# Performance work log

Hardware: AMD Instinct MI355X
Metric: run time of the kernel (lower is better)

## Reference

```python
import jax, jax.numpy as jnp
import numpy as np

B, SEQ, D = 2, 1024, 768
E, H = 8, 3072          # num_experts, expert hidden (mlp_ratio=4)
CAPACITY = 2            # k = CAPACITY * num_tokens


def setup_inputs() -> dict:
    key = jax.random.key(0)
    ks = jax.random.split(key, 6)
    x = jax.random.normal(ks[0], (B, SEQ, D), dtype=jnp.float32)
    gate_weight = jax.random.normal(ks[1], (E, D), dtype=jnp.float32) * 0.006
    w1 = jax.random.normal(ks[2], (E, D, H), dtype=jnp.float32) * (1.0 / np.sqrt(D))
    b1 = jnp.zeros((E, H), dtype=jnp.float32)
    w2 = jax.random.normal(ks[3], (E, H, D), dtype=jnp.float32) * (1.0 / np.sqrt(H))
    b2 = jnp.zeros((E, D), dtype=jnp.float32)
    return {"x": x, "gate_weight": gate_weight, "w1": w1, "b1": b1, "w2": w2, "b2": b2}


def reference(x, gate_weight, w1, b1, w2, b2):
    Bb, s, d = x.shape
    xf = x.reshape(-1, d)                     # [S, D]
    S = xf.shape[0]
    k = S * CAPACITY
    logits = xf @ gate_weight.T               # [S, E]
    scores = jax.nn.softmax(logits, axis=-1).T  # [E, S]
    # flattened top-k over all (expert, token) pairs -> sparse gate matrix
    vals, idx = jax.lax.top_k(scores.reshape(-1), k)
    gate = jnp.zeros((E * S,), dtype=x.dtype).at[idx].add(vals).reshape(E, S)
    # expert MLPs (GELU-tanh) applied per expert; zero gate entries kill
    # non-routed (expert, token) pairs -> same math as gather/MLP/scatter.
    h = jax.nn.gelu(jnp.einsum('sd,edh->esh', xf, w1) + b1[:, None, :], approximate=True)
    out = jnp.einsum('esh,ehd->esd', h, w2) + b2[:, None, :]   # [E, S, D]
    y = jnp.einsum('es,esd->sd', gate, out)    # weighted combine + sum over experts
    return y.reshape(Bb, s, d)
```

## Files before the change

kernel.cpp:

```cpp
#include <hip/hip_runtime.h>
#include <math.h>

#define S_TOK 2048
#define NEXP  8
#define DDIM  768
#define HDIM  3072
#define KSEL  4096
#define NT_MAX 40

typedef __attribute__((ext_vector_type(8))) short short8;
typedef __attribute__((ext_vector_type(4))) float f32x4;

__device__ __forceinline__ unsigned short f2bf(float f) {
  unsigned u = __float_as_uint(f);
  u += 0x7fffu + ((u >> 16) & 1u);
  return (unsigned short)(u >> 16);
}

__device__ __forceinline__ float gelu_fast(float v) {
  float u = 0.7978845608028654f * (v + 0.044715f * v * v * v);
  float t = __expf(-2.0f * fabsf(u));
  float th = (1.0f - t) / (1.0f + t);
  th = copysignf(th, u);
  return 0.5f * v * (1.0f + th);
}

__global__ __launch_bounds__(256) void zero_kernel(float* __restrict__ p, int n) {
  int i = blockIdx.x * 256 + threadIdx.x;
  if (i < n) p[i] = 0.f;
}

__global__ __launch_bounds__(256) void convx_kernel(const float* __restrict__ x,
                                                    short* __restrict__ xb) {
  int i = (blockIdx.x * 256 + threadIdx.x) * 8;
  float4 a = *(const float4*)(x + i);
  float4 b = *(const float4*)(x + i + 4);
  short8 v;
  v[0] = (short)f2bf(a.x); v[1] = (short)f2bf(a.y);
  v[2] = (short)f2bf(a.z); v[3] = (short)f2bf(a.w);
  v[4] = (short)f2bf(b.x); v[5] = (short)f2bf(b.y);
  v[6] = (short)f2bf(b.z); v[7] = (short)f2bf(b.w);
  *(short8*)(xb + i) = v;
}

__global__ __launch_bounds__(256) void gate_kernel(
    const float* __restrict__ x, const float* __restrict__ gw,
    float* __restrict__ scores)
{
  int tid  = threadIdx.x;
  int lane = tid & 63;
  int wid  = tid >> 6;
  int token = blockIdx.x * 4 + wid;
  const float* xr = x + (size_t)token * DDIM;

  float acc[NEXP];
#pragma unroll
  for (int e = 0; e < NEXP; ++e) acc[e] = 0.f;

  for (int d = lane; d < DDIM; d += 64) {
    float xv = xr[d];
#pragma unroll
    for (int e = 0; e < NEXP; ++e) acc[e] += xv * gw[e * DDIM + d];
  }
#pragma unroll
  for (int e = 0; e < NEXP; ++e) {
    for (int off = 32; off; off >>= 1) acc[e] += __shfl_down(acc[e], off, 64);
  }
  if (lane == 0) {
    float m = acc[0];
#pragma unroll
    for (int e = 1; e < NEXP; ++e) m = fmaxf(m, acc[e]);
    float p[NEXP], s = 0.f;
#pragma unroll
    for (int e = 0; e < NEXP; ++e) { p[e] = expf(acc[e] - m); s += p[e]; }
    float inv = 1.0f / s;
#pragma unroll
    for (int e = 0; e < NEXP; ++e) scores[e * S_TOK + token] = p[e] * inv;
  }
}

__device__ unsigned block_scan_excl(unsigned v, volatile unsigned* wsum) {
  int tid = threadIdx.x, lane = tid & 63, wid = tid >> 6;
  __syncthreads();
  unsigned x = v;
#pragma unroll
  for (int off = 1; off < 64; off <<= 1) {
    unsigned t = __shfl_up(x, off, 64);
    if (lane >= off) x += t;
  }
  if (lane == 63) wsum[wid] = x;
  __syncthreads();
  if (tid < 64) {
    unsigned w = (lane < 16) ? wsum[lane] : 0u;
#pragma unroll
    for (int off = 1; off < 16; off <<= 1) {
      unsigned t = __shfl_up(w, off, 64);
      if (lane >= off) w += t;
    }
    if (lane < 16) wsum[lane] = w;
  }
  __syncthreads();
  unsigned woff = (wid > 0) ? wsum[wid - 1] : 0u;
  return woff + (x - v);
}

__global__ __launch_bounds__(1024) void select_kernel(
    const float* __restrict__ scores,
    int* __restrict__ tokenlist, float* __restrict__ slotgate,
    int* __restrict__ offsets, int* __restrict__ tilemap)
{
  __shared__ unsigned cnt;
  __shared__ unsigned wsum[16];
  __shared__ int soff[8];
  int tid = threadIdx.x;
  int base = tid * 16;

  float sv[16]; unsigned key[16];
#pragma unroll
  for (int j = 0; j < 16; ++j) {
    sv[j] = scores[base + j];
    key[j] = __float_as_uint(sv[j]);
  }

  unsigned lo = 0, hi = 0x3F800000u;
  while (lo < hi) {
    unsigned mid = lo + ((hi - lo + 1) >> 1);
    if (tid == 0) cnt = 0;
    __syncthreads();
    unsigned c = 0;
#pragma unroll
    for (int j = 0; j < 16; ++j) c += (key[j] >= mid) ? 1u : 0u;
    for (int off = 32; off; off >>= 1) c += __shfl_down(c, off, 64);
    if ((tid & 63) == 0) atomicAdd(&cnt, c);
    __syncthreads();
    unsigned tot = cnt;
    __syncthreads();
    if (tot >= (unsigned)KSEL) lo = mid; else hi = mid - 1;
  }
  unsigned V = lo;

  if (tid == 0) cnt = 0;
  __syncthreads();
  {
    unsigned c = 0;
#pragma unroll
    for (int j = 0; j < 16; ++j) c += (key[j] > V) ? 1u : 0u;
    for (int off = 32; off; off >>= 1) c += __shfl_down(c, off, 64);
    if ((tid & 63) == 0) atomicAdd(&cnt, c);
  }
  __syncthreads();
  int need = KSEL - (int)cnt;
  __syncthreads();

  unsigned tloc = 0;
#pragma unroll
  for (int j = 0; j < 16; ++j) tloc += (key[j] == V) ? 1u : 0u;
  unsigned texcl = block_scan_excl(tloc, wsum);

  unsigned selmask = 0, sloc = 0, trun = texcl;
#pragma unroll
  for (int j = 0; j < 16; ++j) {
    bool f;
    if (key[j] > V) f = true;
    else if (key[j] == V) { f = ((int)trun < need); ++trun; }
    else f = false;
    if (f) { selmask |= (1u << j); ++sloc; }
  }
  unsigned sexcl = block_scan_excl(sloc, wsum);

  if ((tid & 127) == 0) soff[tid >> 7] = (int)sexcl;
  __syncthreads();
  if (tid == 0) {
    int nt = 0;
#pragma unroll
    for (int e = 0; e < NEXP; ++e) {
      offsets[e] = soff[e];
      int rows = ((e == NEXP - 1) ? KSEL : soff[e + 1]) - soff[e];
      int t = (rows + 127) >> 7;
      for (int i = 0; i < t; ++i) tilemap[nt++] = (e << 16) | i;
    }
    offsets[NEXP] = KSEL;
    for (int i = nt; i < NT_MAX; ++i) tilemap[i] = -1;
  }

  unsigned p = sexcl;
#pragma unroll
  for (int j = 0; j < 16; ++j) {
    int i = base + j;
    if (selmask & (1u << j)) {
      tokenlist[p] = i & (S_TOK - 1);
      slotgate[p] = sv[j];
      ++p;
    }
  }
}

template <int MODE>
__global__ __launch_bounds__(256) void moe_mfma(
    const short* __restrict__ Abase, const float* __restrict__ W,
    const float* __restrict__ bias, void* __restrict__ outp,
    const int* __restrict__ offsets, const int* __restrict__ tokenlist,
    const float* __restrict__ slotgate, const int* __restrict__ tilemap,
    int chunk_base, int K, int N, int klen)
{
  const int tinfo = tilemap[chunk_base + blockIdx.y];
  if (tinfo < 0) return;
  const int e = tinfo >> 16;
  const int tloc = tinfo & 0xffff;
  const int r0 = offsets[e];
  const int rows = offsets[e + 1] - r0;
  const int rowbase = tloc << 7;
  int vr = rows - rowbase; if (vr > 128) vr = 128;
  const int colbase = (int)blockIdx.x << 7;
  const int lbuf = (int)blockIdx.y << 7;
  const int split = (int)blockIdx.z;
  const int kb = split * klen;

  __shared__ short Ab[128 * 40];
  __shared__ short Bb[128 * 40];

  const int tid = threadIdx.x;
  const int lane = tid & 63;
  const int wid = tid >> 6;
  const int wr = (wid >> 1) << 6;
  const int wc = (wid & 1) << 6;
  const int l15 = lane & 15;
  const int lq = lane >> 4;

  const int ar = tid >> 1;
  const int ak = (tid & 1) << 4;
  const short* arow;
  {
    int cr = (ar < vr) ? ar : (vr - 1);
    if (MODE == 1) arow = Abase + (size_t)tokenlist[r0 + rowbase + cr] * DDIM;
    else           arow = Abase + (size_t)(lbuf + cr) * HDIM;
  }
  const int bn = tid & 127;
  const int bk = (tid >> 7) << 4;
  const float* wcol = W + (size_t)e * K * N + colbase + bn;

  f32x4 acc[4][4];
#pragma unroll
  for (int i = 0; i < 4; ++i)
#pragma unroll
    for (int j = 0; j < 4; ++j) acc[i][j] = (f32x4){0.f, 0.f, 0.f, 0.f};

  short8 av0, av1;
  float bw[16];
  {
    const short* ap = arow + kb + ak;
    av0 = *(const short8*)(ap);
    av1 = *(const short8*)(ap + 8);
    const float* wp = wcol + (size_t)(kb + bk) * N;
#pragma unroll
    for (int j = 0; j < 16; ++j) bw[j] = wp[(size_t)j * N];
  }

  for (int k0 = 0; k0 < klen; k0 += 32) {
    __syncthreads();
    *(short8*)&Ab[ar * 40 + ak] = av0;
    *(short8*)&Ab[ar * 40 + ak + 8] = av1;
    {
      short8 b0, b1;
#pragma unroll
      for (int j = 0; j < 8; ++j) {
        b0[j] = (short)f2bf(bw[j]);
        b1[j] = (short)f2bf(bw[j + 8]);
      }
      *(short8*)&Bb[bn * 40 + bk] = b0;
      *(short8*)&Bb[bn * 40 + bk + 8] = b1;
    }
    __syncthreads();
    if (k0 + 32 < klen) {
      const short* ap = arow + kb + k0 + 32 + ak;
      av0 = *(const short8*)(ap);
      av1 = *(const short8*)(ap + 8);
      const float* wp = wcol + (size_t)(kb + k0 + 32 + bk) * N;
#pragma unroll
      for (int j = 0; j < 16; ++j) bw[j] = wp[(size_t)j * N];
    }
    short8 af[4], bfr[4];
#pragma unroll
    for (int i = 0; i < 4; ++i)
      af[i] = *(const short8*)&Ab[(wr + i * 16 + l15) * 40 + lq * 8];
#pragma unroll
    for (int j = 0; j < 4; ++j)
      bfr[j] = *(const short8*)&Bb[(wc + j * 16 + l15) * 40 + lq * 8];
#pragma unroll
    for (int i = 0; i < 4; ++i)
#pragma unroll
      for (int j = 0; j < 4; ++j)
        acc[i][j] = __builtin_amdgcn_mfma_f32_16x16x32_bf16(af[i], bfr[j], acc[i][j], 0, 0, 0);
  }

  if (MODE == 1) {
    short* hb = (short*)outp;
    const float* bp = bias + (size_t)e * N + colbase;
#pragma unroll
    for (int i = 0; i < 4; ++i) {
      int rb = wr + i * 16 + lq * 4;
#pragma unroll
      for (int j = 0; j < 4; ++j) {
        int col = wc + j * 16 + l15;
        float bv = bp[col];
#pragma unroll
        for (int p = 0; p < 4; ++p) {
          int r = rb + p;
          if (r < vr)
            hb[(size_t)(lbuf + r) * HDIM + colbase + col] =
                (short)f2bf(gelu_fast(acc[i][j][p] + bv));
        }
      }
    }
  } else {
    float* y = (float*)outp;
    const float* bp = bias + (size_t)e * N + colbase;
#pragma unroll
    for (int i = 0; i < 4; ++i) {
      int rb = wr + i * 16 + lq * 4;
#pragma unroll
      for (int p = 0; p < 4; ++p) {
        int r = rb + p;
        if (r < vr) {
          int gi = r0 + rowbase + r;
          float g = slotgate[gi];
          float* yrow = y + (size_t)tokenlist[gi] * N + colbase;
#pragma unroll
          for (int j = 0; j < 4; ++j) {
            int col = wc + j * 16 + l15;
            float v = acc[i][j][p] + (split == 0 ? bp[col] : 0.f);
            atomicAdd(&yrow[col], g * v);
          }
        }
      }
    }
  }
}

extern "C" void kernel_launch(void* const* d_in, const int* in_sizes, int n_in,
                              void* d_out, int out_size, void* d_ws, size_t ws_size,
                              hipStream_t stream) {
  const float* x  = (const float*)d_in[0];
  const float* gw = (const float*)d_in[1];
  const float* w1 = (const float*)d_in[2];
  const float* b1 = (const float*)d_in[3];
  const float* w2 = (const float*)d_in[4];
  const float* b2 = (const float*)d_in[5];
  float* y = (float*)d_out;

  char* ws = (char*)d_ws;
  float* scores    = (float*)(ws);
  int*   tokenlist = (int*)(ws + (64 << 10));
  float* slotgate  = (float*)(ws + (80 << 10));
  int*   offsets   = (int*)(ws + (96 << 10));
  int*   tilemap   = (int*)(ws + (96 << 10) + 256);
  short* xbf       = (short*)(ws + (128 << 10));
  short* hbuf      = (short*)(ws + (128 << 10) + (size_t)S_TOK * DDIM * 2);

  const size_t tile_bytes = (size_t)128 * HDIM * 2;
  size_t used = (size_t)(128 << 10) + (size_t)S_TOK * DDIM * 2;
  size_t avail = (ws_size > used) ? ws_size - used : 0;
  int tchunk = (int)(avail / tile_bytes);
  if (tchunk > NT_MAX) tchunk = NT_MAX;
  if (tchunk < 1) tchunk = 1;

  zero_kernel<<<(out_size + 255) / 256, 256, 0, stream>>>(y, out_size);
  convx_kernel<<<S_TOK * DDIM / 2048, 256, 0, stream>>>(x, xbf);
  gate_kernel<<<S_TOK / 4, 256, 0, stream>>>(x, gw, scores);
  select_kernel<<<1, 1024, 0, stream>>>(scores, tokenlist, slotgate, offsets, tilemap);

  for (int t0 = 0; t0 < NT_MAX; t0 += tchunk) {
    int tc = NT_MAX - t0; if (tc > tchunk) tc = tchunk;
    dim3 g1(HDIM / 128, tc, 1);
    moe_mfma<1><<<g1, 256, 0, stream>>>(xbf, w1, b1, hbuf, offsets, tokenlist,
                                        slotgate, tilemap, t0, DDIM, HDIM, DDIM);
    dim3 g2(DDIM / 128, tc, 2);
    moe_mfma<2><<<g2, 256, 0, stream>>>(hbuf, w2, b2, y, offsets, tokenlist,
                                        slotgate, tilemap, t0, HDIM, DDIM, HDIM / 2);
  }
}
```

Before: 204.1 us.

## Replace tilemap chunking with direct expert-indexed grid and double-buffered weight loads

Drops the host-side tile chunk loop and the tilemap array. Each MoE GEMM now launches once over a grid of (expert, column tile, row tile) and exits early for empty row tiles; the H buffer is indexed by slot instead of a chunk-local buffer. The second GEMM goes from a 2-way to a 4-way K split. The K loop is unrolled by two with two register buffers for the fp32 weights so the next global loads overlap the MFMAs. In exchange, the grids are much larger and many blocks exit right away, and the extra K split adds more atomic traffic to the output.

Result: slower. 208.2 us (+2.0%).

```diff
diff --git a/kernel.cpp b/kernel.cpp
--- a/kernel.cpp
+++ b/kernel.cpp
@@ -6,7 +6,6 @@
 #define DDIM  768
 #define HDIM  3072
 #define KSEL  4096
-#define NT_MAX 40
 
 typedef __attribute__((ext_vector_type(8))) short short8;
 typedef __attribute__((ext_vector_type(4))) float f32x4;
@@ -107,11 +106,10 @@
 __global__ __launch_bounds__(1024) void select_kernel(
     const float* __restrict__ scores,
     int* __restrict__ tokenlist, float* __restrict__ slotgate,
-    int* __restrict__ offsets, int* __restrict__ tilemap)
+    int* __restrict__ offsets)
 {
   __shared__ unsigned cnt;
   __shared__ unsigned wsum[16];
-  __shared__ int soff[8];
   int tid = threadIdx.x;
   int base = tid * 16;
 
@@ -168,20 +166,8 @@
   }
   unsigned sexcl = block_scan_excl(sloc, wsum);
 
-  if ((tid & 127) == 0) soff[tid >> 7] = (int)sexcl;
-  __syncthreads();
-  if (tid == 0) {
-    int nt = 0;
-#pragma unroll
-    for (int e = 0; e < NEXP; ++e) {
-      offsets[e] = soff[e];
-      int rows = ((e == NEXP - 1) ? KSEL : soff[e + 1]) - soff[e];
-      int t = (rows + 127) >> 7;
-      for (int i = 0; i < t; ++i) tilemap[nt++] = (e << 16) | i;
-    }
-    offsets[NEXP] = KSEL;
-    for (int i = nt; i < NT_MAX; ++i) tilemap[i] = -1;
-  }
+  if ((tid & 127) == 0) offsets[tid >> 7] = (int)sexcl;
+  if (tid == 0) offsets[NEXP] = KSEL;
 
   unsigned p = sexcl;
 #pragma unroll
@@ -200,23 +186,24 @@
     const short* __restrict__ Abase, const float* __restrict__ W,
     const float* __restrict__ bias, void* __restrict__ outp,
     const int* __restrict__ offsets, const int* __restrict__ tokenlist,
-    const float* __restrict__ slotgate, const int* __restrict__ tilemap,
-    int chunk_base, int K, int N, int klen)
+    const float* __restrict__ slotgate)
 {
-  const int tinfo = tilemap[chunk_base + blockIdx.y];
-  if (tinfo < 0) return;
-  const int e = tinfo >> 16;
-  const int tloc = tinfo & 0xffff;
+  const int e = (int)blockIdx.x;
+  const int K = (MODE == 1) ? DDIM : HDIM;
+  const int N = (MODE == 1) ? HDIM : DDIM;
+  const int tile  = (MODE == 1) ? (int)blockIdx.z : ((int)blockIdx.z >> 2);
+  const int split = (MODE == 1) ? 0 : ((int)blockIdx.z & 3);
+  const int klen  = 768;
+  const int kb = split * klen;
+
   const int r0 = offsets[e];
   const int rows = offsets[e + 1] - r0;
-  const int rowbase = tloc << 7;
+  const int rowbase = tile << 7;
+  if (rowbase >= rows) return;
   int vr = rows - rowbase; if (vr > 128) vr = 128;
-  const int colbase = (int)blockIdx.x << 7;
-  const int lbuf = (int)blockIdx.y << 7;
-  const int split = (int)blockIdx.z;
-  const int kb = split * klen;
-
-  __shared__ short Ab[128 * 40];
+  const int colbase = (int)blockIdx.y << 7;
+
+  __shared__ short As[128 * 40];
   __shared__ short Bb[128 * 40];
 
   const int tid = threadIdx.x;
@@ -233,7 +220,7 @@
   {
     int cr = (ar < vr) ? ar : (vr - 1);
     if (MODE == 1) arow = Abase + (size_t)tokenlist[r0 + rowbase + cr] * DDIM;
-    else           arow = Abase + (size_t)(lbuf + cr) * HDIM;
+    else           arow = Abase + (size_t)(r0 + rowbase + cr) * HDIM + kb;
   }
   const int bn = tid & 127;
   const int bk = (tid >> 7) << 4;
@@ -246,51 +233,77 @@
     for (int j = 0; j < 4; ++j) acc[i][j] = (f32x4){0.f, 0.f, 0.f, 0.f};
 
   short8 av0, av1;
-  float bw[16];
+  float bwA[16], bwB[16];
   {
-    const short* ap = arow + kb + ak;
+    const short* ap = arow + ak;
     av0 = *(const short8*)(ap);
     av1 = *(const short8*)(ap + 8);
-    const float* wp = wcol + (size_t)(kb + bk) * N;
-#pragma unroll
-    for (int j = 0; j < 16; ++j) bw[j] = wp[(size_t)j * N];
-  }
-
-  for (int k0 = 0; k0 < klen; k0 += 32) {
-    __syncthreads();
-    *(short8*)&Ab[ar * 40 + ak] = av0;
-    *(short8*)&Ab[ar * 40 + ak + 8] = av1;
-    {
-      short8 b0, b1;
-#pragma unroll
-      for (int j = 0; j < 8; ++j) {
-        b0[j] = (short)f2bf(bw[j]);
-        b1[j] = (short)f2bf(bw[j + 8]);
-      }
-      *(short8*)&Bb[bn * 40 + bk] = b0;
-      *(short8*)&Bb[bn * 40 + bk + 8] = b1;
-    }
-    __syncthreads();
-    if (k0 + 32 < klen) {
-      const short* ap = arow + kb + k0 + 32 + ak;
-      av0 = *(const short8*)(ap);
-      av1 = *(const short8*)(ap + 8);
-      const float* wp = wcol + (size_t)(kb + k0 + 32 + bk) * N;
-#pragma unroll
-      for (int j = 0; j < 16; ++j) bw[j] = wp[(size_t)j * N];
-    }
-    short8 af[4], bfr[4];
-#pragma unroll
-    for (int i = 0; i < 4; ++i)
-      af[i] = *(const short8*)&Ab[(wr + i * 16 + l15) * 40 + lq * 8];
-#pragma unroll
-    for (int j = 0; j < 4; ++j)
-      bfr[j] = *(const short8*)&Bb[(wc + j * 16 + l15) * 40 + lq * 8];
-#pragma unroll
-    for (int i = 0; i < 4; ++i)
-#pragma unroll
-      for (int j = 0; j < 4; ++j)
-        acc[i][j] = __builtin_amdgcn_mfma_f32_16x16x32_bf16(af[i], bfr[j], acc[i][j], 0, 0, 0);
+    const float* wpA = wcol + (size_t)(kb + bk) * N;
+    const float* wpB = wcol + (size_t)(kb + 32 + bk) * N;
+#pragma unroll
+    for (int j = 0; j < 16; ++j) bwA[j] = wpA[(size_t)j * N];
+#pragma unroll
+    for (int j = 0; j < 16; ++j) bwB[j] = wpB[(size_t)j * N];
+  }
+
+#define WRITE_LDS(BW)                                            \
+  {                                                              \
+    *(short8*)&As[ar * 40 + ak] = av0;                           \
+    *(short8*)&As[ar * 40 + ak + 8] = av1;                       \
+    short8 b0, b1;                                               \
+    _Pragma("unroll")                                            \
+    for (int m = 0; m < 8; ++m) {                                \
+      b0[m] = (short)f2bf(BW[m]);                                \
+      b1[m] = (short)f2bf(BW[m + 8]);                            \
+    }                                                            \
+    *(short8*)&Bb[bn * 40 + bk] = b0;                            \
+    *(short8*)&Bb[bn * 40 + bk + 8] = b1;                        \
+  }
+
+#define LOAD_A(KN)                                               \
+  {                                                              \
+    const short* ap = arow + (KN) + ak;                          \
+    av0 = *(const short8*)(ap);                                  \
+    av1 = *(const short8*)(ap + 8);                              \
+  }
+
+#define LOAD_B(BW, KN)                                           \
+  {                                                              \
+    const float* wp = wcol + (size_t)(kb + (KN) + bk) * N;       \
+    _Pragma("unroll")                                            \
+    for (int j = 0; j < 16; ++j) BW[j] = wp[(size_t)j * N];      \
+  }
+
+#define FRAG_MFMA()                                              \
+  {                                                              \
+    short8 af[4], bfr[4];                                        \
+    _Pragma("unroll")                                            \
+    for (int i = 0; i < 4; ++i)                                  \
+      af[i] = *(const short8*)&As[(wr + i * 16 + l15) * 40 + lq * 8]; \
+    _Pragma("unroll")                                            \
+    for (int j = 0; j < 4; ++j)                                  \
+      bfr[j] = *(const short8*)&Bb[(wc + j * 16 + l15) * 40 + lq * 8]; \
+    _Pragma("unroll")                                            \
+    for (int i = 0; i < 4; ++i)                                  \
+      _Pragma("unroll")                                          \
+      for (int j = 0; j < 4; ++j)                                \
+        acc[i][j] = __builtin_amdgcn_mfma_f32_16x16x32_bf16(af[i], bfr[j], acc[i][j], 0, 0, 0); \
+  }
+
+#pragma unroll 1
+  for (int k0 = 0; k0 < klen; k0 += 64) {
+    __syncthreads();
+    WRITE_LDS(bwA);
+    __syncthreads();
+    LOAD_A(k0 + 32);
+    { int kn = k0 + 64; if (kn >= klen) kn = k0; LOAD_B(bwA, kn); }
+    FRAG_MFMA();
+    __syncthreads();
+    WRITE_LDS(bwB);
+    __syncthreads();
+    { int kn = k0 + 64; if (kn >= klen) kn = k0; LOAD_A(kn); }
+    { int kn = k0 + 96; if (kn >= klen) kn = k0; LOAD_B(bwB, kn); }
+    FRAG_MFMA();
   }
 
   if (MODE == 1) {
@@ -302,13 +315,13 @@
 #pragma unroll
       for (int j = 0; j < 4; ++j) {
         int col = wc + j * 16 + l15;
-        float bv = bp[col];
+        float bvv = bp[col];
 #pragma unroll
         for (int p = 0; p < 4; ++p) {
           int r = rb + p;
           if (r < vr)
-            hb[(size_t)(lbuf + r) * HDIM + colbase + col] =
-                (short)f2bf(gelu_fast(acc[i][j][p] + bv));
+            hb[(size_t)(r0 + rowbase + r) * HDIM + colbase + col] =
+                (short)f2bf(gelu_fast(acc[i][j][p] + bvv));
         }
       }
     }
@@ -353,29 +366,16 @@
   int*   tokenlist = (int*)(ws + (64 << 10));
   float* slotgate  = (float*)(ws + (80 << 10));
   int*   offsets   = (int*)(ws + (96 << 10));
-  int*   tilemap   = (int*)(ws + (96 << 10) + 256);
   short* xbf       = (short*)(ws + (128 << 10));
   short* hbuf      = (short*)(ws + (128 << 10) + (size_t)S_TOK * DDIM * 2);
-
-  const size_t tile_bytes = (size_t)128 * HDIM * 2;
-  size_t used = (size_t)(128 << 10) + (size_t)S_TOK * DDIM * 2;
-  size_t avail = (ws_size > used) ? ws_size - used : 0;
-  int tchunk = (int)(avail / tile_bytes);
-  if (tchunk > NT_MAX) tchunk = NT_MAX;
-  if (tchunk < 1) tchunk = 1;
 
   zero_kernel<<<(out_size + 255) / 256, 256, 0, stream>>>(y, out_size);
   convx_kernel<<<S_TOK * DDIM / 2048, 256, 0, stream>>>(x, xbf);
   gate_kernel<<<S_TOK / 4, 256, 0, stream>>>(x, gw, scores);
-  select_kernel<<<1, 1024, 0, stream>>>(scores, tokenlist, slotgate, offsets, tilemap);
-
-  for (int t0 = 0; t0 < NT_MAX; t0 += tchunk) {
-    int tc = NT_MAX - t0; if (tc > tchunk) tc = tchunk;
-    dim3 g1(HDIM / 128, tc, 1);
-    moe_mfma<1><<<g1, 256, 0, stream>>>(xbf, w1, b1, hbuf, offsets, tokenlist,
-                                        slotgate, tilemap, t0, DDIM, HDIM, DDIM);
-    dim3 g2(DDIM / 128, tc, 2);
-    moe_mfma<2><<<g2, 256, 0, stream>>>(hbuf, w2, b2, y, offsets, tokenlist,
-                                        slotgate, tilemap, t0, HDIM, DDIM, HDIM / 2);
-  }
-}
+  select_kernel<<<1, 1024, 0, stream>>>(scores, tokenlist, slotgate, offsets);
+
+  dim3 g1(NEXP, HDIM / 128, 16);
+  moe_mfma<1><<<g1, 256, 0, stream>>>(xbf, w1, b1, hbuf, offsets, tokenlist, slotgate);
+  dim3 g2(NEXP, DDIM / 128, 64);
+  moe_mfma<2><<<g2, 256, 0, stream>>>(hbuf, w2, b2, y, offsets, tokenlist, slotgate);
+}
```
